# Optimization experiments

Measured on AMD Instinct MI355X. Metric: run time of the kernel, lower is better.

The kernel has to match this reference:

```python
import jax, jax.numpy as jnp
import numpy as np

NUM_HEADS = 16


def setup_inputs() -> dict:
    key = jax.random.key(0)
    ks = jax.random.split(key, 6)
    B, N, M, C = 2, 2048, 2048, 1024
    return {
        "reference_data": jax.random.normal(ks[0], (B, N, C), dtype=jnp.float32),
        "target_data": jax.random.normal(ks[1], (B, M, C), dtype=jnp.float32),
        "Wq": jax.random.normal(ks[2], (C, C), dtype=jnp.float32) * (C ** -0.5),
        "Wkv": jax.random.normal(ks[3], (C, 2 * C), dtype=jnp.float32) * (C ** -0.5),
        "Wproj": jax.random.normal(ks[4], (C, C), dtype=jnp.float32) * (C ** -0.5),
        "bproj": jnp.zeros((C,), dtype=jnp.float32),
    }


def reference(reference_data, target_data, Wq, Wkv, Wproj, bproj):
    B, N, C = reference_data.shape
    M = target_data.shape[1]
    H = NUM_HEADS
    hd = C // H
    scale = hd ** -0.5
    # k, v from reference: [B, N, 2, H, hd] -> two [B, H, N, hd]
    kv = (reference_data @ Wkv).reshape(B, N, 2, H, hd)
    k = jnp.transpose(kv[:, :, 0], (0, 2, 1, 3))  # [B,H,N,hd]
    v = jnp.transpose(kv[:, :, 1], (0, 2, 1, 3))  # [B,H,N,hd]
    # q from target: [B, H, M, hd]
    q = jnp.transpose((target_data @ Wq).reshape(B, M, H, hd), (0, 2, 1, 3))
    attn = jnp.einsum("bhid,bhjd->bhij", q, k) * scale  # [B,H,M,N]
    attn = jax.nn.softmax(attn, axis=-1)
    x = jnp.einsum("bhij,bhjd->bhid", attn, v)  # [B,H,M,hd]
    x = jnp.transpose(x, (0, 2, 1, 3)).reshape(B, M, C)
    return x @ Wproj + bproj
```

## Files before the change

kernel.cpp:

```cpp
#include <hip/hip_runtime.h>
#include <hip/hip_bf16.h>
#include <stdint.h>

#define SEQ   2048
#define CH    1024
#define NH    16
#define HD    64

typedef short bf8 __attribute__((ext_vector_type(8)));
typedef short bf4 __attribute__((ext_vector_type(4)));
typedef float f4  __attribute__((ext_vector_type(4)));
typedef unsigned short u16;

#define GAS(p) ((const __attribute__((address_space(1))) void*)(p))
#define LAS(p) ((__attribute__((address_space(3))) void*)(p))

__device__ __forceinline__ u16 f2bf(float f) {
  uint32_t u = __float_as_uint(f);
  u += 0x7fffu + ((u >> 16) & 1u);
  return (u16)(u >> 16);
}

__device__ __forceinline__ uint32_t pk2bf(float a, float b) {
  float2 f; f.x = a; f.y = b;
  __hip_bfloat162 h = __float22bfloat162_rn(f);
  union { __hip_bfloat162 h; uint32_t u; } cv; cv.h = h;
  return cv.u;
}

__device__ __forceinline__ f4 MFMA32(bf8 a, bf8 b, f4 c) {
  return __builtin_amdgcn_mfma_f32_16x16x32_bf16(a, b, c, 0, 0, 0);
}

__device__ __forceinline__ f4 MFMA16(bf4 a, bf4 b, f4 c) {
#if __has_builtin(__builtin_amdgcn_mfma_f32_16x16x16_bf16)
  return __builtin_amdgcn_mfma_f32_16x16x16_bf16(a, b, c, 0, 0, 0);
#elif __has_builtin(__builtin_amdgcn_mfma_f32_16x16x16bf16_1k)
  return __builtin_amdgcn_mfma_f32_16x16x16bf16_1k(a, b, c, 0, 0, 0);
#else
  f4 d = c;
  asm volatile("v_mfma_f32_16x16x16_bf16 %0, %1, %2, %0"
               : "+v"(d) : "v"(a), "v"(b));
  return d;
#endif
}

__global__ void cvt2_bf16(const float* __restrict__ a, u16* __restrict__ oa,
                          const float* __restrict__ b, u16* __restrict__ ob) {
  int blk = blockIdx.x;
  const float* in; u16* out;
  if (blk < 4096) { in = a; out = oa; } else { in = b; out = ob; blk -= 4096; }
  int i = (blk * 256 + threadIdx.x) * 4;
  float4 f = *reinterpret_cast<const float4*>(in + i);
  ushort4 o;
  o.x = f2bf(f.x); o.y = f2bf(f.y); o.z = f2bf(f.z); o.w = f2bf(f.w);
  *reinterpret_cast<ushort4*>(out + i) = o;
}

__global__ void transp_all(const float* __restrict__ Wq, u16* __restrict__ Wqt,
                           const float* __restrict__ Wkv, u16* __restrict__ Wkvt,
                           const float* __restrict__ Wp, u16* __restrict__ Wpt) {
  __shared__ float tile[32][33];
  int x = blockIdx.x;
  const float* in; u16* out; int N;
  if (x < 32)       { in = Wq;  out = Wqt;  N = CH;     }
  else if (x < 96)  { in = Wkv; out = Wkvt; N = 2 * CH; x -= 32; }
  else              { in = Wp;  out = Wpt;  N = CH;     x -= 96; }
  const int K = CH;
  int bn = x * 32, bk = blockIdx.y * 32;
  int tx = threadIdx.x, ty = threadIdx.y;
  #pragma unroll
  for (int i = ty; i < 32; i += 8)
    tile[i][tx] = in[(size_t)(bk + i) * N + bn + tx];
  __syncthreads();
  #pragma unroll
  for (int i = ty; i < 32; i += 8)
    out[(size_t)(bn + i) * K + bk + tx] = f2bf(tile[tx][i]);
}

__global__ __launch_bounds__(256, 2)
void gemm_qkv(const u16* __restrict__ tgtb, const u16* __restrict__ refb,
              const u16* __restrict__ Wqt, const u16* __restrict__ Wkvt,
              u16* __restrict__ qb, u16* __restrict__ karr, u16* __restrict__ varr)
{
  __shared__ __align__(16) u16 As[2][4096];
  __shared__ __align__(16) u16 Bs[2][4096];
  const int tid = threadIdx.x;
  const int lane = tid & 63, wave = tid >> 6;
  const int l16 = lane & 15, q = lane >> 4;
  const bool isQ = blockIdx.x >= 16;
  const u16* A  = isQ ? tgtb : refb;
  const u16* Bt = isQ ? Wqt : Wkvt;
  const int n0 = (isQ ? (blockIdx.x - 16) : blockIdx.x) * 128;
  const int m0 = blockIdx.y * 128;
  const int wm = (wave >> 1) * 64, wn = (wave & 1) * 64;
  const int Kdim = CH;
  const int c = tid, c2 = tid + 256;
  const int ar = c >> 2, ac = (c & 3) << 3, ar2 = c2 >> 2, ac2 = (c2 & 3) << 3;

  f4 acc[4][4] = {};

  #define STAGE_G(buf, k0)                                                      \
    { __builtin_amdgcn_global_load_lds(                                         \
          GAS(&A[(size_t)(m0 + ar) * Kdim + (k0) + ac]),                        \
          LAS(&As[buf][c << 3]), 16, 0, 0);                                     \
      __builtin_amdgcn_global_load_lds(                                         \
          GAS(&A[(size_t)(m0 + ar2) * Kdim + (k0) + ac2]),                      \
          LAS(&As[buf][c2 << 3]), 16, 0, 0);                                    \
      __builtin_amdgcn_global_load_lds(                                         \
          GAS(&Bt[(size_t)(n0 + ar) * Kdim + (k0) + ac]),                       \
          LAS(&Bs[buf][c << 3]), 16, 0, 0);                                     \
      __builtin_amdgcn_global_load_lds(                                         \
          GAS(&Bt[(size_t)(n0 + ar2) * Kdim + (k0) + ac2]),                     \
          LAS(&Bs[buf][c2 << 3]), 16, 0, 0); }

  STAGE_G(0, 0);
  for (int kk = 0; kk < 32; ++kk) {
    __syncthreads();
    if (kk < 31) STAGE_G((kk + 1) & 1, (kk + 1) * 32);
    const u16* as = As[kk & 1];
    const u16* bs = Bs[kk & 1];
    bf8 a[4], b[4];
    #pragma unroll
    for (int i = 0; i < 4; ++i)
      a[i] = *reinterpret_cast<const bf8*>(&as[(wm + i * 16 + l16) * 32 + q * 8]);
    #pragma unroll
    for (int j = 0; j < 4; ++j)
      b[j] = *reinterpret_cast<const bf8*>(&bs[(wn + j * 16 + l16) * 32 + q * 8]);
    #pragma unroll
    for (int i = 0; i < 4; ++i)
      #pragma unroll
      for (int j = 0; j < 4; ++j)
        acc[i][j] = MFMA32(a[i], b[j], acc[i][j]);
  }
  #undef STAGE_G

  #pragma unroll
  for (int i = 0; i < 4; ++i) {
    const int mbase = m0 + wm + i * 16 + q * 4;
    const int b = mbase >> 11, ns0 = mbase & (SEQ - 1);
    #pragma unroll
    for (int j = 0; j < 4; ++j) {
      const int n = n0 + wn + j * 16 + l16;
      if (isQ) {
        int h = n >> 6, d = n & 63;
        #pragma unroll
        for (int r = 0; r < 4; ++r)
          qb[(size_t)((b * NH + h) * SEQ + ns0 + r) * HD + d] =
              f2bf(acc[i][j][r] * 0.1803368801f);
      } else if (n < CH) {
        int h = n >> 6, d = n & 63;
        size_t base = (size_t)(b * NH + h) * SEQ * HD;
        int off = (((ns0 >> 4) * 2 + (d >> 5)) * 4 + ((d >> 3) & 3)) * 128
                  + (d & 7);
        #pragma unroll
        for (int r = 0; r < 4; ++r)
          karr[base + off + ((ns0 + r) & 15) * 8] = f2bf(acc[i][j][r]);
      } else {
        int c2v = n - CH, h = c2v >> 6, d = c2v & 63;
        size_t base = (size_t)(b * NH + h) * SEQ * HD;
        int off = (((ns0 >> 4) * 4 + (d >> 4)) * 4 + ((ns0 >> 2) & 3)) * 64
                  + (d & 15) * 4;
        ushort4 st;
        st.x = f2bf(acc[i][j][0]); st.y = f2bf(acc[i][j][1]);
        st.z = f2bf(acc[i][j][2]); st.w = f2bf(acc[i][j][3]);
        *reinterpret_cast<ushort4*>(&varr[base + off]) = st;
      }
    }
  }
}

__global__ __launch_bounds__(256, 2)
void gemm_proj(const u16* __restrict__ A, const u16* __restrict__ Bt,
               float* __restrict__ fo, const float* __restrict__ bias)
{
  __shared__ __align__(16) u16 As[2][4096];
  __shared__ __align__(16) u16 Bs[2][4096];
  const int tid = threadIdx.x;
  const int lane = tid & 63, wave = tid >> 6;
  const int l16 = lane & 15, q = lane >> 4;
  const int m0 = blockIdx.y * 128, n0 = blockIdx.x * 128;
  const int wm = (wave >> 1) * 64, wn = (wave & 1) * 64;
  const int Kdim = CH;
  const int c = tid, c2 = tid + 256;
  const int ar = c >> 2, ac = (c & 3) << 3, ar2 = c2 >> 2, ac2 = (c2 & 3) << 3;

  f4 acc[4][4] = {};

  #define STAGE_P(buf, k0)                                                      \
    { __builtin_amdgcn_global_load_lds(                                         \
          GAS(&A[(size_t)(m0 + ar) * Kdim + (k0) + ac]),                        \
          LAS(&As[buf][c << 3]), 16, 0, 0);                                     \
      __builtin_amdgcn_global_load_lds(                                         \
          GAS(&A[(size_t)(m0 + ar2) * Kdim + (k0) + ac2]),                      \
          LAS(&As[buf][c2 << 3]), 16, 0, 0);                                    \
      __builtin_amdgcn_global_load_lds(                                         \
          GAS(&Bt[(size_t)(n0 + ar) * Kdim + (k0) + ac]),                       \
          LAS(&Bs[buf][c << 3]), 16, 0, 0);                                     \
      __builtin_amdgcn_global_load_lds(                                         \
          GAS(&Bt[(size_t)(n0 + ar2) * Kdim + (k0) + ac2]),                     \
          LAS(&Bs[buf][c2 << 3]), 16, 0, 0); }

  STAGE_P(0, 0);
  for (int kk = 0; kk < 32; ++kk) {
    __syncthreads();
    if (kk < 31) STAGE_P((kk + 1) & 1, (kk + 1) * 32);
    const u16* as = As[kk & 1];
    const u16* bs = Bs[kk & 1];
    bf8 a[4], b[4];
    #pragma unroll
    for (int i = 0; i < 4; ++i)
      a[i] = *reinterpret_cast<const bf8*>(&as[(wm + i * 16 + l16) * 32 + q * 8]);
    #pragma unroll
    for (int j = 0; j < 4; ++j)
      b[j] = *reinterpret_cast<const bf8*>(&bs[(wn + j * 16 + l16) * 32 + q * 8]);
    #pragma unroll
    for (int i = 0; i < 4; ++i)
      #pragma unroll
      for (int j = 0; j < 4; ++j)
        acc[i][j] = MFMA32(a[i], b[j], acc[i][j]);
  }
  #undef STAGE_P

  #pragma unroll
  for (int i = 0; i < 4; ++i) {
    const int mbase = m0 + wm + i * 16 + q * 4;
    #pragma unroll
    for (int j = 0; j < 4; ++j) {
      const int n = n0 + wn + j * 16 + l16;
      #pragma unroll
      for (int r = 0; r < 4; ++r)
        fo[(size_t)(mbase + r) * CH + n] = acc[i][j][r] + bias[n];
    }
  }
}

__global__ __launch_bounds__(512, 4)
void attn(const u16* __restrict__ Q, const u16* __restrict__ Karr,
          const u16* __restrict__ Varr, u16* __restrict__ X)
{
  __shared__ __align__(16) u16 Ks[2][8192];
  __shared__ __align__(16) u16 Vs[2][8192];
  const int tid = threadIdx.x;
  const int lane = tid & 63;
  const int l16 = lane & 15, q = lane >> 4;
  const int bh = blockIdx.y;
  const int m0 = blockIdx.x * 128;
  const int wm = (tid >> 6) * 16;

  const u16* Qb = Q    + (size_t)bh * SEQ * HD;
  const u16* Kb = Karr + (size_t)bh * SEQ * HD;
  const u16* Vb = Varr + (size_t)bh * SEQ * HD;

  bf8 qf[2];
  #pragma unroll
  for (int ks = 0; ks < 2; ++ks)
    qf[ks] = *reinterpret_cast<const bf8*>(
        &Qb[(size_t)(m0 + wm + l16) * HD + ks * 32 + q * 8]);

  const short one_bf = 0x3F80;
  const bf4 ones = {one_bf, one_bf, one_bf, one_bf};

  f4 o[4] = {};
  f4 ds = {};

  #define STAGE_A(buf, t)                                                       \
    { const u16* kg = Kb + (size_t)(t) * 8192;                                  \
      const u16* vg = Vb + (size_t)(t) * 8192;                                  \
      _Pragma("unroll")                                                         \
      for (int s = 0; s < 2; ++s) {                                             \
        int cc = tid + s * 512;                                                 \
        __builtin_amdgcn_global_load_lds(GAS(kg + cc * 8),                      \
                                         LAS(&Ks[buf][cc * 8]), 16, 0, 0);      \
        __builtin_amdgcn_global_load_lds(GAS(vg + cc * 8),                      \
                                         LAS(&Vs[buf][cc * 8]), 16, 0, 0);      \
      } }

  STAGE_A(0, 0);
  for (int t = 0; t < SEQ / 128; ++t) {
    __syncthreads();
    if (t < SEQ / 128 - 1) STAGE_A((t + 1) & 1, t + 1);
    const u16* ks = Ks[t & 1];
    const u16* vs = Vs[t & 1];

    bf4 pa[8];
    #pragma unroll
    for (int j = 0; j < 8; ++j) {
      bf8 kf0 = *reinterpret_cast<const bf8*>(&ks[((j * 2 + 0) * 4 + q) * 128 + l16 * 8]);
      bf8 kf1 = *reinterpret_cast<const bf8*>(&ks[((j * 2 + 1) * 4 + q) * 128 + l16 * 8]);
      f4 z = {};
      z = MFMA32(kf0, qf[0], z);
      z = MFMA32(kf1, qf[1], z);
      union { bf4 v; uint32_t u[2]; } w;
      w.u[0] = pk2bf(exp2f(z[0]), exp2f(z[1]));
      w.u[1] = pk2bf(exp2f(z[2]), exp2f(z[3]));
      pa[j] = w.v;
    }

    #pragma unroll
    for (int j = 0; j < 8; ++j) {
      ds = MFMA16(pa[j], ones, ds);
      #pragma unroll
      for (int dt = 0; dt < 4; ++dt) {
        bf4 vf = *reinterpret_cast<const bf4*>(&vs[((j * 4 + dt) * 4 + q) * 64 + l16 * 4]);
        o[dt] = MFMA16(pa[j], vf, o[dt]);
      }
    }
  }
  #undef STAGE_A

  const int b = bh >> 4, h = bh & (NH - 1);
  #pragma unroll
  for (int r = 0; r < 4; ++r) {
    float ir = 1.0f / ds[r];
    int m = m0 + wm + q * 4 + r;
    #pragma unroll
    for (int dt = 0; dt < 4; ++dt) {
      int d = dt * 16 + l16;
      X[(size_t)(b * SEQ + m) * CH + h * HD + d] = f2bf(o[dt][r] * ir);
    }
  }
}

extern "C" void kernel_launch(void* const* d_in, const int* in_sizes, int n_in,
                              void* d_out, int out_size, void* d_ws, size_t ws_size,
                              hipStream_t stream) {
  const float* ref   = (const float*)d_in[0];
  const float* tgt   = (const float*)d_in[1];
  const float* Wq    = (const float*)d_in[2];
  const float* Wkv   = (const float*)d_in[3];
  const float* Wproj = (const float*)d_in[4];
  const float* bproj = (const float*)d_in[5];
  float* out = (float*)d_out;

  char* ws = (char*)d_ws;
  u16* refb = (u16*)(ws);
  u16* tgtb = (u16*)(ws + (8  << 20));
  u16* Wqt  = (u16*)(ws + (16 << 20));
  u16* Wkvt = (u16*)(ws + (18 << 20));
  u16* Wpt  = (u16*)(ws + (22 << 20));
  u16* qb   = (u16*)(ws + (24 << 20));
  u16* karr = (u16*)(ws + (32 << 20));
  u16* varr = (u16*)(ws + (40 << 20));
  u16* xb   = (u16*)(ws + (48 << 20));

  cvt2_bf16<<<8192, 256, 0, stream>>>(ref, refb, tgt, tgtb);
  transp_all<<<dim3(128, 32), dim3(32, 8), 0, stream>>>(Wq, Wqt, Wkv, Wkvt, Wproj, Wpt);

  gemm_qkv<<<dim3(24, 32), 256, 0, stream>>>(tgtb, refb, Wqt, Wkvt, qb, karr, varr);

  attn<<<dim3(16, 32), 512, 0, stream>>>(qb, karr, varr, xb);

  gemm_proj<<<dim3(8, 32), 256, 0, stream>>>(xb, Wpt, out, bproj);
}
```

Measured before the change: 222.9 us.

## Merge prep kernels, retile projection GEMM, widen V fragment loads in attention

Merges the input bf16 conversion and the weight transpose into a single prep launch, dropping one kernel launch. The projection GEMM moves to 64-row tiles so it launches twice as many blocks, giving better occupancy across CUs. The V layout written by the QKV GEMM changes so attention can read one 8-wide bf16 fragment and split it across two MFMAs, halving its LDS read instructions. The QKV GEMM's launch bound hint rises to 3 blocks per CU, which may add register pressure.

Result: faster. 214.1 us (-4.0%).

```diff
diff --git a/kernel.cpp b/kernel.cpp
--- a/kernel.cpp
+++ b/kernel.cpp
@@ -45,30 +45,33 @@
 #endif
 }
 
-__global__ void cvt2_bf16(const float* __restrict__ a, u16* __restrict__ oa,
-                          const float* __restrict__ b, u16* __restrict__ ob) {
+__global__ void prep(const float* __restrict__ ref, u16* __restrict__ refb,
+                     const float* __restrict__ tgt, u16* __restrict__ tgtb,
+                     const float* __restrict__ Wq, u16* __restrict__ Wqt,
+                     const float* __restrict__ Wkv, u16* __restrict__ Wkvt,
+                     const float* __restrict__ Wp, u16* __restrict__ Wpt) {
+  __shared__ float tile[32][33];
   int blk = blockIdx.x;
-  const float* in; u16* out;
-  if (blk < 4096) { in = a; out = oa; } else { in = b; out = ob; blk -= 4096; }
-  int i = (blk * 256 + threadIdx.x) * 4;
-  float4 f = *reinterpret_cast<const float4*>(in + i);
-  ushort4 o;
-  o.x = f2bf(f.x); o.y = f2bf(f.y); o.z = f2bf(f.z); o.w = f2bf(f.w);
-  *reinterpret_cast<ushort4*>(out + i) = o;
-}
-
-__global__ void transp_all(const float* __restrict__ Wq, u16* __restrict__ Wqt,
-                           const float* __restrict__ Wkv, u16* __restrict__ Wkvt,
-                           const float* __restrict__ Wp, u16* __restrict__ Wpt) {
-  __shared__ float tile[32][33];
-  int x = blockIdx.x;
+  int t = threadIdx.x;
+  if (blk < 8192) {
+    const float* in; u16* out;
+    if (blk < 4096) { in = ref; out = refb; } else { in = tgt; out = tgtb; blk -= 4096; }
+    int i = (blk * 256 + t) * 4;
+    float4 f = *reinterpret_cast<const float4*>(in + i);
+    ushort4 o;
+    o.x = f2bf(f.x); o.y = f2bf(f.y); o.z = f2bf(f.z); o.w = f2bf(f.w);
+    *reinterpret_cast<ushort4*>(out + i) = o;
+    return;
+  }
+  blk -= 8192;
+  int x = blk & 127, by = blk >> 7;
   const float* in; u16* out; int N;
   if (x < 32)       { in = Wq;  out = Wqt;  N = CH;     }
   else if (x < 96)  { in = Wkv; out = Wkvt; N = 2 * CH; x -= 32; }
   else              { in = Wp;  out = Wpt;  N = CH;     x -= 96; }
   const int K = CH;
-  int bn = x * 32, bk = blockIdx.y * 32;
-  int tx = threadIdx.x, ty = threadIdx.y;
+  int bn = x * 32, bk = by * 32;
+  int tx = t & 31, ty = t >> 5;
   #pragma unroll
   for (int i = ty; i < 32; i += 8)
     tile[i][tx] = in[(size_t)(bk + i) * N + bn + tx];
@@ -78,7 +81,7 @@
     out[(size_t)(bn + i) * K + bk + tx] = f2bf(tile[tx][i]);
 }
 
-__global__ __launch_bounds__(256, 2)
+__global__ __launch_bounds__(256, 3)
 void gemm_qkv(const u16* __restrict__ tgtb, const u16* __restrict__ refb,
               const u16* __restrict__ Wqt, const u16* __restrict__ Wkvt,
               u16* __restrict__ qb, u16* __restrict__ karr, u16* __restrict__ varr)
@@ -159,8 +162,8 @@
       } else {
         int c2v = n - CH, h = c2v >> 6, d = c2v & 63;
         size_t base = (size_t)(b * NH + h) * SEQ * HD;
-        int off = (((ns0 >> 4) * 4 + (d >> 4)) * 4 + ((ns0 >> 2) & 3)) * 64
-                  + (d & 15) * 4;
+        int off = (((ns0 >> 4) * 2 + (d >> 5)) * 4 + ((ns0 >> 2) & 3)) * 128
+                  + (d & 15) * 8 + ((d >> 4) & 1) * 4;
         ushort4 st;
         st.x = f2bf(acc[i][j][0]); st.y = f2bf(acc[i][j][1]);
         st.z = f2bf(acc[i][j][2]); st.w = f2bf(acc[i][j][3]);
@@ -174,26 +177,37 @@
 void gemm_proj(const u16* __restrict__ A, const u16* __restrict__ Bt,
                float* __restrict__ fo, const float* __restrict__ bias)
 {
-  __shared__ __align__(16) u16 As[2][4096];
+  __shared__ __align__(16) u16 As[2][2048];
   __shared__ __align__(16) u16 Bs[2][4096];
   const int tid = threadIdx.x;
   const int lane = tid & 63, wave = tid >> 6;
   const int l16 = lane & 15, q = lane >> 4;
-  const int m0 = blockIdx.y * 128, n0 = blockIdx.x * 128;
-  const int wm = (wave >> 1) * 64, wn = (wave & 1) * 64;
+  const int m0 = blockIdx.y * 64, n0 = blockIdx.x * 128;
+  const int wm = (wave >> 1) * 32, wn = (wave & 1) * 64;
   const int Kdim = CH;
   const int c = tid, c2 = tid + 256;
   const int ar = c >> 2, ac = (c & 3) << 3, ar2 = c2 >> 2, ac2 = (c2 & 3) << 3;
 
-  f4 acc[4][4] = {};
+  f4 acc[2][4] = {};
 
   #define STAGE_P(buf, k0)                                                      \
     { __builtin_amdgcn_global_load_lds(                                         \
-          GAS(&A[(size_t)(m0 + ar) * Kdim + (k0) + ac]),                        \
+          GAS(&A[(size_t)(m0 + (ar >> 1)) * Kdim + (k0) + ((c & 7) << 2) * 2]), \
+          LAS(&As[buf][(c & 255) << 3]), 16, 0, 0);                             \
+      __builtin_amdgcn_global_load_lds(                                         \
+          GAS(&Bt[(size_t)(n0 + ar) * Kdim + (k0) + ac]),                       \
+          LAS(&Bs[buf][c << 3]), 16, 0, 0);                                     \
+      __builtin_amdgcn_global_load_lds(                                         \
+          GAS(&Bt[(size_t)(n0 + ar2) * Kdim + (k0) + ac2]),                     \
+          LAS(&Bs[buf][c2 << 3]), 16, 0, 0); }
+
+  #undef STAGE_P
+  const int aar = c >> 2;
+  const int aac = (c & 3) << 3;
+  #define STAGE_P(buf, k0)                                                      \
+    { __builtin_amdgcn_global_load_lds(                                         \
+          GAS(&A[(size_t)(m0 + aar) * Kdim + (k0) + aac]),                      \
           LAS(&As[buf][c << 3]), 16, 0, 0);                                     \
-      __builtin_amdgcn_global_load_lds(                                         \
-          GAS(&A[(size_t)(m0 + ar2) * Kdim + (k0) + ac2]),                      \
-          LAS(&As[buf][c2 << 3]), 16, 0, 0);                                    \
       __builtin_amdgcn_global_load_lds(                                         \
           GAS(&Bt[(size_t)(n0 + ar) * Kdim + (k0) + ac]),                       \
           LAS(&Bs[buf][c << 3]), 16, 0, 0);                                     \
@@ -207,15 +221,15 @@
     if (kk < 31) STAGE_P((kk + 1) & 1, (kk + 1) * 32);
     const u16* as = As[kk & 1];
     const u16* bs = Bs[kk & 1];
-    bf8 a[4], b[4];
-    #pragma unroll
-    for (int i = 0; i < 4; ++i)
+    bf8 a[2], b[4];
+    #pragma unroll
+    for (int i = 0; i < 2; ++i)
       a[i] = *reinterpret_cast<const bf8*>(&as[(wm + i * 16 + l16) * 32 + q * 8]);
     #pragma unroll
     for (int j = 0; j < 4; ++j)
       b[j] = *reinterpret_cast<const bf8*>(&bs[(wn + j * 16 + l16) * 32 + q * 8]);
     #pragma unroll
-    for (int i = 0; i < 4; ++i)
+    for (int i = 0; i < 2; ++i)
       #pragma unroll
       for (int j = 0; j < 4; ++j)
         acc[i][j] = MFMA32(a[i], b[j], acc[i][j]);
@@ -223,7 +237,7 @@
   #undef STAGE_P
 
   #pragma unroll
-  for (int i = 0; i < 4; ++i) {
+  for (int i = 0; i < 2; ++i) {
     const int mbase = m0 + wm + i * 16 + q * 4;
     #pragma unroll
     for (int j = 0; j < 4; ++j) {
@@ -301,9 +315,12 @@
     for (int j = 0; j < 8; ++j) {
       ds = MFMA16(pa[j], ones, ds);
       #pragma unroll
-      for (int dt = 0; dt < 4; ++dt) {
-        bf4 vf = *reinterpret_cast<const bf4*>(&vs[((j * 4 + dt) * 4 + q) * 64 + l16 * 4]);
-        o[dt] = MFMA16(pa[j], vf, o[dt]);
+      for (int dh = 0; dh < 2; ++dh) {
+        bf8 vv = *reinterpret_cast<const bf8*>(&vs[((j * 2 + dh) * 4 + q) * 128 + l16 * 8]);
+        bf4 v0 = __builtin_shufflevector(vv, vv, 0, 1, 2, 3);
+        bf4 v1 = __builtin_shufflevector(vv, vv, 4, 5, 6, 7);
+        o[dh * 2 + 0] = MFMA16(pa[j], v0, o[dh * 2 + 0]);
+        o[dh * 2 + 1] = MFMA16(pa[j], v1, o[dh * 2 + 1]);
       }
     }
   }
@@ -344,12 +361,11 @@
   u16* varr = (u16*)(ws + (40 << 20));
   u16* xb   = (u16*)(ws + (48 << 20));
 
-  cvt2_bf16<<<8192, 256, 0, stream>>>(ref, refb, tgt, tgtb);
-  transp_all<<<dim3(128, 32), dim3(32, 8), 0, stream>>>(Wq, Wqt, Wkv, Wkvt, Wproj, Wpt);
+  prep<<<12288, 256, 0, stream>>>(ref, refb, tgt, tgtb, Wq, Wqt, Wkv, Wkvt, Wproj, Wpt);
 
   gemm_qkv<<<dim3(24, 32), 256, 0, stream>>>(tgtb, refb, Wqt, Wkvt, qb, karr, varr);
 
   attn<<<dim3(16, 32), 512, 0, stream>>>(qb, karr, varr, xb);
 
-  gemm_proj<<<dim3(8, 32), 256, 0, stream>>>(xb, Wpt, out, bproj);
-}
+  gemm_proj<<<dim3(8, 64), 256, 0, stream>>>(xb, Wpt, out, bproj);
+}
```
